# Kernel tuning notes

Hardware: AMD Instinct MI355X
Metric: run time of the kernel (lower is better)

The kernel has to match this reference:

```python
import jax, jax.numpy as jnp
import numpy as np

B, C, W, H = 16, 512, 32, 32


def spatial_shift1(y):
    # y: [B, W, H, C]; quartile-wise shifts with edge rows/cols left unchanged
    c = y.shape[-1]
    cq = c // 4
    p0 = jnp.concatenate([y[:, :1, :, 0*cq:1*cq], y[:, :-1, :, 0*cq:1*cq]], axis=1)  # w <- w-1
    p1 = jnp.concatenate([y[:, 1:, :, 1*cq:2*cq], y[:, -1:, :, 1*cq:2*cq]], axis=1)  # w <- w+1
    p2 = jnp.concatenate([y[:, :, :1, 2*cq:3*cq], y[:, :, :-1, 2*cq:3*cq]], axis=2)  # h <- h-1
    p3 = jnp.concatenate([y[:, :, 1:, 3*cq:], y[:, :, -1:, 3*cq:]], axis=2)          # h <- h+1
    return jnp.concatenate([p0, p1, p2, p3], axis=-1)


def spatial_shift2(y):
    # same as shift1 with w/h roles swapped
    c = y.shape[-1]
    cq = c // 4
    p0 = jnp.concatenate([y[:, :, :1, 0*cq:1*cq], y[:, :, :-1, 0*cq:1*cq]], axis=2)  # h <- h-1
    p1 = jnp.concatenate([y[:, :, 1:, 1*cq:2*cq], y[:, :, -1:, 1*cq:2*cq]], axis=2)  # h <- h+1
    p2 = jnp.concatenate([y[:, :1, :, 2*cq:3*cq], y[:, :-1, :, 2*cq:3*cq]], axis=1)  # w <- w-1
    p3 = jnp.concatenate([y[:, 1:, :, 3*cq:], y[:, -1:, :, 3*cq:]], axis=1)          # w <- w+1
    return jnp.concatenate([p0, p1, p2, p3], axis=-1)


def setup_inputs() -> dict:
    key = jax.random.key(0)
    ks = jax.random.split(key, 9)
    s = 0.02
    return {
        "x": jax.random.normal(ks[0], (B, C, W, H), dtype=jnp.float32),
        "w1": jax.random.normal(ks[1], (3 * C, C), dtype=jnp.float32) * s,
        "b1": jax.random.normal(ks[2], (3 * C,), dtype=jnp.float32) * s,
        "wa": jax.random.normal(ks[3], (C, C), dtype=jnp.float32) * s,
        "ba": jax.random.normal(ks[4], (C,), dtype=jnp.float32) * s,
        "wb": jax.random.normal(ks[5], (3 * C, C), dtype=jnp.float32) * s,
        "bb": jax.random.normal(ks[6], (3 * C,), dtype=jnp.float32) * s,
        "w2": jax.random.normal(ks[7], (C, C), dtype=jnp.float32) * s,
        "b2": jax.random.normal(ks[8], (C,), dtype=jnp.float32) * s,
    }


def reference(x, w1, b1, wa, ba, wb, bb, w2, b2):
    c = x.shape[1]
    xp = jnp.transpose(x, (0, 2, 3, 1))                     # [B, W, H, C]
    y = jnp.einsum("bwhc,oc->bwho", xp, w1) + b1            # [B, W, H, 3C]
    x1 = spatial_shift1(y[..., :c])
    x2 = spatial_shift2(y[..., c:2 * c])
    x3 = y[..., 2 * c:]
    # SplitAttention: descriptor a = sum over branches and spatial positions
    a = jnp.sum(x1 + x2 + x3, axis=(1, 2))                  # [B, C]
    hat = jax.nn.gelu(a @ wa.T + ba, approximate=False) @ wb.T + bb  # [B, 3C]
    bar = jax.nn.softmax(hat.reshape(-1, 3, c), axis=1)     # softmax over k=3
    g = bar[:, :, None, None, :]                            # [B, 3, 1, 1, C]
    out = g[:, 0] * x1 + g[:, 1] * x2 + g[:, 2] * x3        # [B, W, H, C]
    z = jnp.einsum("bwhc,oc->bwho", out, w2) + b2           # [B, W, H, C]
    return jnp.transpose(z, (0, 3, 1, 2))                   # [B, C, W, H]
```

## Files before the change

### kernel.cpp

```cpp
#include <hip/hip_runtime.h>
#include <stdint.h>

typedef __bf16 bf16x8 __attribute__((ext_vector_type(8)));
typedef float f32x4 __attribute__((ext_vector_type(4)));

#define B_ 16
#define C_ 512
#define S_ 1024
#define N1 1536

__device__ inline unsigned short f2b(float f) {
    unsigned int u = __builtin_bit_cast(unsigned int, f);
    unsigned int lsb = (u >> 16) & 1u;
    u += 0x7fffu + lsb;
    return (unsigned short)(u >> 16);
}
__device__ inline float b2f(unsigned int s) {
    unsigned int u = (s & 0xffffu) << 16;
    return __builtin_bit_cast(float, u);
}

__device__ inline void gl_lds16(const unsigned short* g, unsigned short* l) {
    __builtin_amdgcn_global_load_lds(
        (const __attribute__((address_space(1))) void*)(g),
        (__attribute__((address_space(3))) void*)(l),
        16, 0, 0);
}

__global__ __launch_bounds__(256) void transpose_convert_x(
    const float* __restrict__ x, unsigned short* __restrict__ xT,
    const float* __restrict__ w1, const float* __restrict__ w2,
    unsigned short* __restrict__ w1b, unsigned short* __restrict__ w2b,
    float* __restrict__ sums)
{
    int t = threadIdx.x;
    if (blockIdx.z == 16) {
        int base = (blockIdx.y * 16 + blockIdx.x) * 256 + t;
        for (int i = base; i < 292864; i += 32768) {
            if (i < 196608) {
                float4 v = ((const float4*)w1)[i];
                ((ushort4*)w1b)[i] = make_ushort4(f2b(v.x), f2b(v.y), f2b(v.z), f2b(v.w));
            } else if (i < 262144) {
                int j = i - 196608;
                float4 v = ((const float4*)w2)[j];
                ((ushort4*)w2b)[j] = make_ushort4(f2b(v.x), f2b(v.y), f2b(v.z), f2b(v.w));
            } else {
                int j = i - 262144;
                ((float4*)sums)[j] = make_float4(0.f, 0.f, 0.f, 0.f);
            }
        }
        return;
    }
    __shared__ float tile[64][68];
    int b = blockIdx.z;
    int c0 = blockIdx.y * 64;
    int s0 = blockIdx.x * 64;
    int r = t >> 2, q4 = t & 3;
    const float* xp = x + ((size_t)(b * C_ + c0 + r)) * S_ + s0;
#pragma unroll
    for (int k = 0; k < 4; k++) {
        float4 v = ((const float4*)xp)[q4 + 4 * k];
        *(float4*)&tile[r][(q4 + 4 * k) * 4] = v;
    }
    __syncthreads();
    int sr = t >> 2;
    unsigned short* op = xT + ((size_t)(b * S_ + s0 + sr)) * C_ + c0;
#pragma unroll
    for (int kk = 0; kk < 2; kk++) {
        int chunk = q4 + 4 * kk;
        unsigned int pz[4];
#pragma unroll
        for (int i2 = 0; i2 < 4; i2++) {
            int c = chunk * 8 + i2 * 2;
            pz[i2] = (unsigned int)f2b(tile[c][sr]) | ((unsigned int)f2b(tile[c + 1][sr]) << 16);
        }
        *(uint4*)&op[chunk * 8] = make_uint4(pz[0], pz[1], pz[2], pz[3]);
    }
}

template <bool TRANS_OUT, bool DO_SUMS>
__global__ __launch_bounds__(512, 2) void gemm_2ph(
    const unsigned short* __restrict__ A,
    const unsigned short* __restrict__ Wt,
    const float* __restrict__ bias,
    void* __restrict__ Cout,
    float* __restrict__ Tsum, float* __restrict__ H0, float* __restrict__ H31,
    float* __restrict__ C0, float* __restrict__ C31)
{
    __shared__ __align__(16) unsigned short lds[49152];
    const int tid = threadIdx.x;
    const int lane = tid & 63, wid = tid >> 6;
    const int wm = (wid >> 2) * 64;
    const int wn = (wid & 3) * 64;
    const int quad = lane >> 4, l16 = lane & 15;
    const int m0 = blockIdx.x * 128;
    const int n0 = blockIdx.y * 256;
    const unsigned short* Ab = A + (size_t)m0 * 512;
    const unsigned short* Bb = Wt + (size_t)n0 * 512;

    f32x4 acc[4][4] = {};

    auto stageA = [&](int T) {
        unsigned short* dst = &lds[(T & 1) * 8192];
#pragma unroll
        for (int i = 0; i < 2; i++) {
            int ch = i * 512 + tid;
            int r = ch >> 3, kc = ch & 7;
            gl_lds16(Ab + (size_t)r * 512 + T * 64 + ((kc ^ (r & 7)) * 8), dst + ch * 8);
        }
    };
    auto stageB = [&](int T) {
        unsigned short* dst = &lds[16384 + (T & 1) * 16384];
#pragma unroll
        for (int i = 0; i < 4; i++) {
            int ch = i * 512 + tid;
            int r = ch >> 3, kc = ch & 7;
            gl_lds16(Bb + (size_t)r * 512 + T * 64 + ((kc ^ (r & 7)) * 8), dst + ch * 8);
        }
    };

    stageB(0); stageA(0); stageB(1);
    asm volatile("s_waitcnt vmcnt(4)" ::: "memory");
    __builtin_amdgcn_s_barrier();

    for (int T = 0; T < 8; T++) {
        const unsigned short* Asl = &lds[(T & 1) * 8192];
        const unsigned short* Bsl = &lds[16384 + (T & 1) * 16384];
        bf16x8 bfr[4][2], af[2][2];
#pragma unroll
        for (int nt = 0; nt < 4; nt++)
#pragma unroll
            for (int kh = 0; kh < 2; kh++) {
                int rb = wn + nt * 16 + l16;
                bfr[nt][kh] = *(const bf16x8*)&Bsl[rb * 64 + (((kh * 4 + quad) ^ (rb & 7)) * 8)];
            }
#pragma unroll
        for (int mi = 0; mi < 2; mi++)
#pragma unroll
            for (int kh = 0; kh < 2; kh++) {
                int ra = wm + mi * 16 + l16;
                af[mi][kh] = *(const bf16x8*)&Asl[ra * 64 + (((kh * 4 + quad) ^ (ra & 7)) * 8)];
            }
        if (T < 7) stageA(T + 1);
        __builtin_amdgcn_s_barrier();
        asm volatile("s_waitcnt lgkmcnt(0)" ::: "memory");
        __builtin_amdgcn_sched_barrier(0);
        __builtin_amdgcn_s_setprio(1);
#pragma unroll
        for (int mi = 0; mi < 2; mi++)
#pragma unroll
            for (int nt = 0; nt < 4; nt++)
#pragma unroll
                for (int kh = 0; kh < 2; kh++)
                    acc[mi][nt] = __builtin_amdgcn_mfma_f32_16x16x32_bf16(
                        af[mi][kh], bfr[nt][kh], acc[mi][nt], 0, 0, 0);
        __builtin_amdgcn_s_setprio(0);
        __builtin_amdgcn_s_barrier();
#pragma unroll
        for (int mi = 0; mi < 2; mi++)
#pragma unroll
            for (int kh = 0; kh < 2; kh++) {
                int ra = wm + (2 + mi) * 16 + l16;
                af[mi][kh] = *(const bf16x8*)&Asl[ra * 64 + (((kh * 4 + quad) ^ (ra & 7)) * 8)];
            }
        if (T < 6) {
            stageB(T + 2);
            asm volatile("s_waitcnt vmcnt(4)" ::: "memory");
        } else if (T == 6) {
            asm volatile("s_waitcnt vmcnt(0)" ::: "memory");
        }
        __builtin_amdgcn_s_barrier();
        asm volatile("s_waitcnt lgkmcnt(0)" ::: "memory");
        __builtin_amdgcn_sched_barrier(0);
        __builtin_amdgcn_s_setprio(1);
#pragma unroll
        for (int mi = 0; mi < 2; mi++)
#pragma unroll
            for (int nt = 0; nt < 4; nt++)
#pragma unroll
                for (int kh = 0; kh < 2; kh++)
                    acc[2 + mi][nt] = __builtin_amdgcn_mfma_f32_16x16x32_bf16(
                        af[mi][kh], bfr[nt][kh], acc[2 + mi][nt], 0, 0, 0);
        __builtin_amdgcn_s_setprio(0);
        __builtin_amdgcn_s_barrier();
    }

    if (!TRANS_OUT) {
        unsigned short* eb = lds;
#pragma unroll
        for (int mt = 0; mt < 4; mt++)
#pragma unroll
            for (int nt = 0; nt < 4; nt++) {
                int col = wn + nt * 16 + l16;
                float bv = bias[n0 + col];
                int cc = col >> 3, cw = col & 7;
#pragma unroll
                for (int r = 0; r < 4; r++) {
                    int row = wm + mt * 16 + quad * 4 + r;
                    eb[row * 256 + (((cc ^ (row & 7)) << 3) + cw)] = f2b(acc[mt][nt][r] + bv);
                }
            }
        __syncthreads();
        unsigned short* Y = (unsigned short*)Cout;
#pragma unroll
        for (int it = 0; it < 8; it++) {
            int cid = it * 512 + tid;
            int row = cid >> 5, j = cid & 31;
            bf16x8 v = *(const bf16x8*)&eb[row * 256 + ((j ^ (row & 7)) << 3)];
            *(bf16x8*)&Y[(size_t)(m0 + row) * N1 + n0 + j * 8] = v;
        }
    } else {
        float* ef = (float*)lds;
        int b = m0 >> 10, s0r = m0 & 1023;
        float* O = (float*)Cout;
#pragma unroll
        for (int p = 0; p < 2; p++) {
            if (((wid & 3) >> 1) == p) {
#pragma unroll
                for (int mt = 0; mt < 4; mt++)
#pragma unroll
                    for (int nt = 0; nt < 4; nt++) {
                        int nl = wn - p * 128 + nt * 16 + l16;
                        float bv = bias[n0 + p * 128 + nl];
                        int c = (wm >> 2) + mt * 4 + quad;
                        f32x4 v;
#pragma unroll
                        for (int r = 0; r < 4; r++) v[r] = acc[mt][nt][r] + bv;
                        *(f32x4*)&ef[nl * 128 + ((c ^ (nl & 7)) << 2)] = v;
                    }
            }
            __syncthreads();
#pragma unroll
            for (int it = 0; it < 8; it++) {
                int cid = it * 512 + tid;
                int nl = cid >> 5, j = cid & 31;
                f32x4 v = *(const f32x4*)&ef[nl * 128 + ((j ^ (nl & 7)) << 2)];
                *(f32x4*)&O[((size_t)(b * 512 + n0 + p * 128 + nl)) * 1024 + s0r + j * 4] = v;
            }
            if (p == 0) __syncthreads();
        }
    }

    if (DO_SUMS) {
        int b = m0 >> 10;
        int wlo = (m0 & 1023) >> 5;
#pragma unroll
        for (int nt = 0; nt < 4; nt++) {
            int n = n0 + wn + nt * 16 + l16;
            float bv = bias[n];
            float tT = 0.f;
#pragma unroll
            for (int mt = 0; mt < 4; mt++)
#pragma unroll
                for (int r = 0; r < 4; r++) tT += acc[mt][nt][r] + bv;
            tT += __shfl_xor(tT, 16);
            tT += __shfl_xor(tT, 32);
            if (quad == 0) {
                atomicAdd(&Tsum[b * 1536 + n], tT);
                float th0 = acc[0][nt][0] + acc[2][nt][0] + 2.f * bv;
                atomicAdd(&H0[b * 1536 + n], th0);
            }
            if (quad == 3) {
                float th31 = acc[1][nt][3] + acc[3][nt][3] + 2.f * bv;
                atomicAdd(&H31[b * 1536 + n], th31);
            }
            if (wlo == 0 && wm == 0) {
                float tc = 0.f;
#pragma unroll
                for (int mt = 0; mt < 2; mt++)
#pragma unroll
                    for (int r = 0; r < 4; r++) tc += acc[mt][nt][r] + bv;
                tc += __shfl_xor(tc, 16);
                tc += __shfl_xor(tc, 32);
                if (quad == 0) atomicAdd(&C0[b * 1536 + n], tc);
            }
            if (wlo == 28 && wm == 64) {
                float tc = 0.f;
#pragma unroll
                for (int mt = 2; mt < 4; mt++)
#pragma unroll
                    for (int r = 0; r < 4; r++) tc += acc[mt][nt][r] + bv;
                tc += __shfl_xor(tc, 16);
                tc += __shfl_xor(tc, 32);
                if (quad == 0) atomicAdd(&C31[b * 1536 + n], tc);
            }
        }
    }
}

__global__ __launch_bounds__(512, 2) void gemm2_fused(
    const unsigned short* __restrict__ Yg,
    const float* __restrict__ hat,
    const unsigned short* __restrict__ Wt,
    const float* __restrict__ bias,
    float* __restrict__ O)
{
    __shared__ __align__(16) unsigned short As[2 * 8192];
    __shared__ __align__(16) unsigned short Bs[2 * 16384];
    __shared__ float gs[3][512];
    const int tid = threadIdx.x;
    const int lane = tid & 63, wid = tid >> 6;
    const int wm = (wid >> 2) * 64;
    const int wn = (wid & 3) * 64;
    const int quad = lane >> 4, l16 = lane & 15;
    const int m0 = blockIdx.x * 128;
    const int n0 = blockIdx.y * 256;
    const int b = m0 >> 10, s0 = m0 & 1023, w0 = s0 >> 5;
    const int bq = b * 1024;
    const unsigned short* Bb = Wt + (size_t)n0 * 512;
    const int chunk = tid & 7, mpair = tid >> 3;
    const int wA = w0 + ((mpair * 2) >> 5);

    f32x4 acc[4][4] = {};

    {
        int c = tid;
        float h0v = hat[b * 1536 + c];
        float h1v = hat[b * 1536 + 512 + c];
        float h2v = hat[b * 1536 + 1024 + c];
        float mx = fmaxf(h0v, fmaxf(h1v, h2v));
        float e0 = __expf(h0v - mx), e1 = __expf(h1v - mx), e2 = __expf(h2v - mx);
        float inv = 1.0f / (e0 + e1 + e2);
        gs[0][c] = e0 * inv; gs[1][c] = e1 * inv; gs[2][c] = e2 * inv;
    }
    __syncthreads();

    auto stageB = [&](int T) {
        unsigned short* dst = &Bs[(T & 1) * 16384];
#pragma unroll
        for (int i = 0; i < 4; i++) {
            int ch = i * 512 + tid;
            int r = ch >> 3, kc = ch & 7;
            gl_lds16(Bb + (size_t)r * 512 + T * 64 + ((kc ^ (r & 7)) * 8), dst + ch * 8);
        }
    };

    uint4 u1[2], u2[2], u3[2];
    auto issueA = [&](int Tn) {
        int q = Tn >> 1;
        int dw1 = (q == 0) ? -1 : (q == 1) ? 1 : 0;
        int dh1 = (q == 2) ? -1 : (q == 3) ? 1 : 0;
        int dh2 = (q == 0) ? -1 : (q == 1) ? 1 : 0;
        int dw2 = (q == 2) ? -1 : (q == 3) ? 1 : 0;
        int cg = Tn * 64 + chunk * 8;
#pragma unroll
        for (int j = 0; j < 2; j++) {
            int ml = mpair * 2 + j;
            int w = w0 + (ml >> 5), h = ml & 31;
            int r1 = bq + min(max(w + dw1, 0), 31) * 32 + min(max(h + dh1, 0), 31);
            int r2 = bq + min(max(w + dw2, 0), 31) * 32 + min(max(h + dh2, 0), 31);
            int r3 = bq + w * 32 + h;
            u1[j] = *(const uint4*)&Yg[(size_t)r1 * 1536 + cg];
            u2[j] = *(const uint4*)&Yg[(size_t)r2 * 1536 + 512 + cg];
            u3[j] = *(const uint4*)&Yg[(size_t)r3 * 1536 + 1024 + cg];
        }
    };
    auto writeA = [&](int Tn) {
        int cg = Tn * 64 + chunk * 8;
        float g0v[8], g1v[8], g2v[8];
        *(float4*)&g0v[0] = *(const float4*)&gs[0][cg];
        *(float4*)&g0v[4] = *(const float4*)&gs[0][cg + 4];
        *(float4*)&g1v[0] = *(const float4*)&gs[1][cg];
        *(float4*)&g1v[4] = *(const float4*)&gs[1][cg + 4];
        *(float4*)&g2v[0] = *(const float4*)&gs[2][cg];
        *(float4*)&g2v[4] = *(const float4*)&gs[2][cg + 4];
#pragma unroll
        for (int j = 0; j < 2; j++) {
            const unsigned int* a1 = (const unsigned int*)&u1[j];
            const unsigned int* a2 = (const unsigned int*)&u2[j];
            const unsigned int* a3 = (const unsigned int*)&u3[j];
            unsigned int p[4];
#pragma unroll
            for (int k = 0; k < 4; k++) {
                float lo = g0v[2 * k] * b2f(a1[k]) + g1v[2 * k] * b2f(a2[k]) + g2v[2 * k] * b2f(a3[k]);
                float hi = g0v[2 * k + 1] * b2f(a1[k] >> 16) + g1v[2 * k + 1] * b2f(a2[k] >> 16) + g2v[2 * k + 1] * b2f(a3[k] >> 16);
                p[k] = (unsigned int)f2b(lo) | ((unsigned int)f2b(hi) << 16);
            }
            int ml = mpair * 2 + j;
            *(uint4*)&As[(Tn & 1) * 8192 + ml * 64 + ((chunk ^ (ml & 7)) * 8)] = *(const uint4*)p;
        }
    };

    stageB(0);
    issueA(0);
    stageB(1);
    asm volatile("s_waitcnt vmcnt(4)" ::: "memory");
    writeA(0);
    asm volatile("s_waitcnt lgkmcnt(0)" ::: "memory");
    __builtin_amdgcn_s_barrier();

    for (int T = 0; T < 8; T++) {
        const unsigned short* Asl = &As[(T & 1) * 8192];
        const unsigned short* Bsl = &Bs[(T & 1) * 16384];
        bf16x8 bfr[4][2], af[2][2];
#pragma unroll
        for (int nt = 0; nt < 4; nt++)
#pragma unroll
            for (int kh = 0; kh < 2; kh++) {
                int rb = wn + nt * 16 + l16;
                bfr[nt][kh] = *(const bf16x8*)&Bsl[rb * 64 + (((kh * 4 + quad) ^ (rb & 7)) * 8)];
            }
#pragma unroll
        for (int mi = 0; mi < 2; mi++)
#pragma unroll
            for (int kh = 0; kh < 2; kh++) {
                int ra = wm + mi * 16 + l16;
                af[mi][kh] = *(const bf16x8*)&Asl[ra * 64 + (((kh * 4 + quad) ^ (ra & 7)) * 8)];
            }
        if (T < 7) issueA(T + 1);
        __builtin_amdgcn_s_barrier();
        asm volatile("s_waitcnt lgkmcnt(0)" ::: "memory");
        __builtin_amdgcn_sched_barrier(0);
        __builtin_amdgcn_s_setprio(1);
#pragma unroll
        for (int mi = 0; mi < 2; mi++)
#pragma unroll
            for (int nt = 0; nt < 4; nt++)
#pragma unroll
                for (int kh = 0; kh < 2; kh++)
                    acc[mi][nt] = __builtin_amdgcn_mfma_f32_16x16x32_bf16(
                        af[mi][kh], bfr[nt][kh], acc[mi][nt], 0, 0, 0);
        __builtin_amdgcn_s_setprio(0);
        __builtin_amdgcn_s_barrier();
#pragma unroll
        for (int mi = 0; mi < 2; mi++)
#pragma unroll
            for (int kh = 0; kh < 2; kh++) {
                int ra = wm + (2 + mi) * 16 + l16;
                af[mi][kh] = *(const bf16x8*)&Asl[ra * 64 + (((kh * 4 + quad) ^ (ra & 7)) * 8)];
            }
        if (T < 6) stageB(T + 2);
        if (T < 7) {
            if (T < 6) asm volatile("s_waitcnt vmcnt(4)" ::: "memory");
            else       asm volatile("s_waitcnt vmcnt(0)" ::: "memory");
            writeA(T + 1);
        }
        __builtin_amdgcn_s_barrier();
        asm volatile("s_waitcnt lgkmcnt(0)" ::: "memory");
        __builtin_amdgcn_sched_barrier(0);
        __builtin_amdgcn_s_setprio(1);
#pragma unroll
        for (int mi = 0; mi < 2; mi++)
#pragma unroll
            for (int nt = 0; nt < 4; nt++)
#pragma unroll
                for (int kh = 0; kh < 2; kh++)
                    acc[2 + mi][nt] = __builtin_amdgcn_mfma_f32_16x16x32_bf16(
                        af[mi][kh], bfr[nt][kh], acc[2 + mi][nt], 0, 0, 0);
        __builtin_amdgcn_s_setprio(0);
        __builtin_amdgcn_s_barrier();
    }

    float* ef = (float*)Bs;
#pragma unroll
    for (int p = 0; p < 2; p++) {
        if (((wid & 3) >> 1) == p) {
#pragma unroll
            for (int mt = 0; mt < 4; mt++)
#pragma unroll
                for (int nt = 0; nt < 4; nt++) {
                    int nl = wn - p * 128 + nt * 16 + l16;
                    float bv = bias[n0 + p * 128 + nl];
                    int c = (wm >> 2) + mt * 4 + quad;
                    f32x4 v;
#pragma unroll
                    for (int r = 0; r < 4; r++) v[r] = acc[mt][nt][r] + bv;
                    *(f32x4*)&ef[nl * 128 + ((c ^ (nl & 7)) << 2)] = v;
                }
        }
        __syncthreads();
#pragma unroll
        for (int it = 0; it < 8; it++) {
            int cid = it * 512 + tid;
            int nl = cid >> 5, j = cid & 31;
            f32x4 v = *(const f32x4*)&ef[nl * 128 + ((j ^ (nl & 7)) << 2)];
            *(f32x4*)&O[((size_t)(b * 512 + n0 + p * 128 + nl)) * 1024 + s0 + j * 4] = v;
        }
        if (p == 0) __syncthreads();
    }
}

__global__ __launch_bounds__(256) void mlp_layer1(
    const float* __restrict__ sums, const float* __restrict__ wa,
    const float* __restrict__ ba, float* __restrict__ h)
{
    __shared__ float sa[512];
    int b = blockIdx.x >> 7;
    int t = threadIdx.x;
    const float* Tp   = sums;
    const float* H0p  = sums + 24576;
    const float* H31p = sums + 49152;
    const float* C0p  = sums + 73728;
    const float* C31p = sums + 98304;
#pragma unroll
    for (int j = 0; j < 2; j++) {
        int c = t + j * 256;
        int q = c >> 7;
        int n1 = b * 1536 + c;
        float t123 = Tp[n1] + Tp[n1 + 512] + Tp[n1 + 1024];
        float sC1 = C0p[n1] - C31p[n1];
        float sH1 = H0p[n1] - H31p[n1];
        float sC2 = C0p[n1 + 512] - C31p[n1 + 512];
        float sH2 = H0p[n1 + 512] - H31p[n1 + 512];
        float e = (q < 2) ? (sC1 + sH2) : (sH1 + sC2);
        sa[c] = t123 + ((q & 1) ? -e : e);
    }
    __syncthreads();
    int lane = t & 63, wid = t >> 6;
    int o = (blockIdx.x & 127) * 4 + wid;
    const float4* wr = (const float4*)(wa + (size_t)o * 512);
    float4 w0 = wr[lane * 2], w1v = wr[lane * 2 + 1];
    float4 a0 = ((const float4*)sa)[lane * 2], a1 = ((const float4*)sa)[lane * 2 + 1];
    float dot = w0.x * a0.x + w0.y * a0.y + w0.z * a0.z + w0.w * a0.w
              + w1v.x * a1.x + w1v.y * a1.y + w1v.z * a1.z + w1v.w * a1.w;
#pragma unroll
    for (int off = 32; off; off >>= 1) dot += __shfl_down(dot, off);
    if (lane == 0) {
        float v = dot + ba[o];
        h[b * 512 + o] = 0.5f * v * (1.0f + erff(v * 0.7071067811865475f));
    }
}

__global__ __launch_bounds__(256) void mlp_layer2(
    const float* __restrict__ h, const float* __restrict__ wb,
    const float* __restrict__ bb, float* __restrict__ hat)
{
    __shared__ float sh[512];
    int b = blockIdx.x / 96;
    int og = blockIdx.x - b * 96;
    int t = threadIdx.x;
    sh[t] = h[b * 512 + t];
    sh[t + 256] = h[b * 512 + 256 + t];
    __syncthreads();
    int lane = t & 63, wid = t >> 6;
    float4 a0 = ((const float4*)sh)[lane * 2], a1 = ((const float4*)sh)[lane * 2 + 1];
#pragma unroll
    for (int i = 0; i < 4; i++) {
        int o = og * 16 + wid * 4 + i;
        const float4* wr = (const float4*)(wb + (size_t)o * 512);
        float4 w0 = wr[lane * 2], w1 = wr[lane * 2 + 1];
        float dot = w0.x * a0.x + w0.y * a0.y + w0.z * a0.z + w0.w * a0.w
                  + w1.x * a1.x + w1.y * a1.y + w1.z * a1.z + w1.w * a1.w;
#pragma unroll
        for (int off = 32; off; off >>= 1) dot += __shfl_down(dot, off);
        if (lane == 0)
            hat[(size_t)b * 1536 + o] = dot + bb[o];
    }
}

extern "C" void kernel_launch(void* const* d_in, const int* in_sizes, int n_in,
                              void* d_out, int out_size, void* d_ws, size_t ws_size,
                              hipStream_t stream) {
    const float* x  = (const float*)d_in[0];
    const float* w1 = (const float*)d_in[1];
    const float* b1 = (const float*)d_in[2];
    const float* wa = (const float*)d_in[3];
    const float* ba = (const float*)d_in[4];
    const float* wb = (const float*)d_in[5];
    const float* bb = (const float*)d_in[6];
    const float* w2 = (const float*)d_in[7];
    const float* b2 = (const float*)d_in[8];
    float* out = (float*)d_out;

    char* ws = (char*)d_ws;
    unsigned short* xT   = (unsigned short*)(ws);
    unsigned short* w1b  = (unsigned short*)(ws + 16777216);
    unsigned short* w2b  = (unsigned short*)(ws + 18350080);
    unsigned short* y    = (unsigned short*)(ws + 18874368);
    float* sums          = (float*)(ws + 69206016);
    float* h_buf         = (float*)(ws + 69697536);
    float* hat_buf       = (float*)(ws + 69730304);

    float* Tsum = sums;
    float* H0   = sums + 24576;
    float* H31  = sums + 49152;
    float* C0   = sums + 73728;
    float* C31  = sums + 98304;

    transpose_convert_x<<<dim3(16, 8, 17), dim3(256), 0, stream>>>(
        x, xT, w1, w2, w1b, w2b, sums);
    gemm_2ph<false, true><<<dim3(128, 6), dim3(512), 0, stream>>>(
        xT, w1b, b1, (void*)y, Tsum, H0, H31, C0, C31);
    mlp_layer1<<<dim3(2048), dim3(256), 0, stream>>>(sums, wa, ba, h_buf);
    mlp_layer2<<<dim3(1536), dim3(256), 0, stream>>>(h_buf, wb, bb, hat_buf);
    gemm2_fused<<<dim3(128, 2), dim3(512), 0, stream>>>(
        y, hat_buf, w2b, b2, out);
}
```

Baseline: 175.3 us.

## Rewrite first GEMM with 128x128 tiles and register double-buffered fragments

The first projection GEMM moves from 128x256 tiles with 512 threads to 128x128 tiles with 256 threads. The grid becomes 12x128 with N as the fast dimension, so neighbouring blocks share the same A rows. A and B are staged together into LDS two tiles ahead. The next tile's MFMA fragments are preloaded into a second register buffer while the current tile's MFMAs run, to overlap LDS reads with compute. The cost is more register pressure and a full vmcnt(0) wait plus a barrier every iteration, which may cut into the overlap.

```diff
diff --git a/kernel.cpp b/kernel.cpp
--- a/kernel.cpp
+++ b/kernel.cpp
@@ -78,114 +78,93 @@
     }
 }
 
-template <bool TRANS_OUT, bool DO_SUMS>
-__global__ __launch_bounds__(512, 2) void gemm_2ph(
+__global__ __launch_bounds__(256, 2) void gemm1_sb(
     const unsigned short* __restrict__ A,
     const unsigned short* __restrict__ Wt,
     const float* __restrict__ bias,
-    void* __restrict__ Cout,
+    unsigned short* __restrict__ Y,
     float* __restrict__ Tsum, float* __restrict__ H0, float* __restrict__ H31,
     float* __restrict__ C0, float* __restrict__ C31)
 {
-    __shared__ __align__(16) unsigned short lds[49152];
+    __shared__ __align__(16) unsigned short lds[32768];
     const int tid = threadIdx.x;
     const int lane = tid & 63, wid = tid >> 6;
-    const int wm = (wid >> 2) * 64;
-    const int wn = (wid & 3) * 64;
+    const int wm = (wid >> 1) * 64;
+    const int wn = (wid & 1) * 64;
     const int quad = lane >> 4, l16 = lane & 15;
-    const int m0 = blockIdx.x * 128;
-    const int n0 = blockIdx.y * 256;
+    const int n0 = blockIdx.x * 128;
+    const int m0 = blockIdx.y * 128;
     const unsigned short* Ab = A + (size_t)m0 * 512;
     const unsigned short* Bb = Wt + (size_t)n0 * 512;
 
     f32x4 acc[4][4] = {};
-
-    auto stageA = [&](int T) {
-        unsigned short* dst = &lds[(T & 1) * 8192];
-#pragma unroll
-        for (int i = 0; i < 2; i++) {
-            int ch = i * 512 + tid;
+    bf16x8 afs[2][4][2], bfs[2][4][2];
+
+    auto stage = [&](int T) {
+        unsigned short* dA = &lds[(T & 1) * 8192];
+        unsigned short* dB = &lds[16384 + (T & 1) * 8192];
+#pragma unroll
+        for (int i = 0; i < 4; i++) {
+            int ch = i * 256 + tid;
             int r = ch >> 3, kc = ch & 7;
-            gl_lds16(Ab + (size_t)r * 512 + T * 64 + ((kc ^ (r & 7)) * 8), dst + ch * 8);
+            size_t go = (size_t)r * 512 + T * 64 + ((kc ^ (r & 7)) * 8);
+            gl_lds16(Ab + go, dA + ch * 8);
+            gl_lds16(Bb + go, dB + ch * 8);
         }
     };
-    auto stageB = [&](int T) {
-        unsigned short* dst = &lds[16384 + (T & 1) * 16384];
-#pragma unroll
-        for (int i = 0; i < 4; i++) {
-            int ch = i * 512 + tid;
-            int r = ch >> 3, kc = ch & 7;
-            gl_lds16(Bb + (size_t)r * 512 + T * 64 + ((kc ^ (r & 7)) * 8), dst + ch * 8);
-        }
-    };
-
-    stageB(0); stageA(0); stageB(1);
-    asm volatile("s_waitcnt vmcnt(4)" ::: "memory");
+
+    stage(0); stage(1);
+    asm volatile("s_waitcnt vmcnt(8)" ::: "memory");
     __builtin_amdgcn_s_barrier();
-
+    {
+        const unsigned short* Asl = &lds[0];
+        const unsigned short* Bsl = &lds[16384];
+#pragma unroll
+        for (int mt = 0; mt < 4; mt++)
+#pragma unroll
+            for (int kh = 0; kh < 2; kh++) {
+                int ra = wm + mt * 16 + l16;
+                afs[0][mt][kh] = *(const bf16x8*)&Asl[ra * 64 + (((kh * 4 + quad) ^ (ra & 7)) * 8)];
+                int rb = wn + mt * 16 + l16;
+                bfs[0][mt][kh] = *(const bf16x8*)&Bsl[rb * 64 + (((kh * 4 + quad) ^ (rb & 7)) * 8)];
+            }
+    }
+
+#pragma unroll
     for (int T = 0; T < 8; T++) {
-        const unsigned short* Asl = &lds[(T & 1) * 8192];
-        const unsigned short* Bsl = &lds[16384 + (T & 1) * 16384];
-        bf16x8 bfr[4][2], af[2][2];
-#pragma unroll
-        for (int nt = 0; nt < 4; nt++)
-#pragma unroll
-            for (int kh = 0; kh < 2; kh++) {
-                int rb = wn + nt * 16 + l16;
-                bfr[nt][kh] = *(const bf16x8*)&Bsl[rb * 64 + (((kh * 4 + quad) ^ (rb & 7)) * 8)];
-            }
-#pragma unroll
-        for (int mi = 0; mi < 2; mi++)
-#pragma unroll
-            for (int kh = 0; kh < 2; kh++) {
-                int ra = wm + mi * 16 + l16;
-                af[mi][kh] = *(const bf16x8*)&Asl[ra * 64 + (((kh * 4 + quad) ^ (ra & 7)) * 8)];
-            }
-        if (T < 7) stageA(T + 1);
+        const int cur = T & 1, nxt = cur ^ 1;
+        asm volatile("s_waitcnt lgkmcnt(0)" ::: "memory");
+        asm volatile("s_waitcnt vmcnt(0)" ::: "memory");
         __builtin_amdgcn_s_barrier();
-        asm volatile("s_waitcnt lgkmcnt(0)" ::: "memory");
+        if (T < 6) stage(T + 2);
+        if (T < 7) {
+            const unsigned short* Asl = &lds[nxt * 8192];
+            const unsigned short* Bsl = &lds[16384 + nxt * 8192];
+#pragma unroll
+            for (int mt = 0; mt < 4; mt++)
+#pragma unroll
+                for (int kh = 0; kh < 2; kh++) {
+                    int ra = wm + mt * 16 + l16;
+                    afs[nxt][mt][kh] = *(const bf16x8*)&Asl[ra * 64 + (((kh * 4 + quad) ^ (ra & 7)) * 8)];
+                    int rb = wn + mt * 16 + l16;
+                    bfs[nxt][mt][kh] = *(const bf16x8*)&Bsl[rb * 64 + (((kh * 4 + quad) ^ (rb & 7)) * 8)];
+                }
+        }
         __builtin_amdgcn_sched_barrier(0);
         __builtin_amdgcn_s_setprio(1);
 #pragma unroll
-        for (int mi = 0; mi < 2; mi++)
+        for (int mt = 0; mt < 4; mt++)
 #pragma unroll
             for (int nt = 0; nt < 4; nt++)
 #pragma unroll
                 for (int kh = 0; kh < 2; kh++)
-                    acc[mi][nt] = __builtin_amdgcn_mfma_f32_16x16x32_bf16(
-                        af[mi][kh], bfr[nt][kh], acc[mi][nt], 0, 0, 0);
+                    acc[mt][nt] = __builtin_amdgcn_mfma_f32_16x16x32_bf16(
+                        afs[cur][mt][kh], bfs[cur][nt][kh], acc[mt][nt], 0, 0, 0);
         __builtin_amdgcn_s_setprio(0);
-        __builtin_amdgcn_s_barrier();
-#pragma unroll
-        for (int mi = 0; mi < 2; mi++)
-#pragma unroll
-            for (int kh = 0; kh < 2; kh++) {
-                int ra = wm + (2 + mi) * 16 + l16;
-                af[mi][kh] = *(const bf16x8*)&Asl[ra * 64 + (((kh * 4 + quad) ^ (ra & 7)) * 8)];
-            }
-        if (T < 6) {
-            stageB(T + 2);
-            asm volatile("s_waitcnt vmcnt(4)" ::: "memory");
-        } else if (T == 6) {
-            asm volatile("s_waitcnt vmcnt(0)" ::: "memory");
-        }
-        __builtin_amdgcn_s_barrier();
-        asm volatile("s_waitcnt lgkmcnt(0)" ::: "memory");
-        __builtin_amdgcn_sched_barrier(0);
-        __builtin_amdgcn_s_setprio(1);
-#pragma unroll
-        for (int mi = 0; mi < 2; mi++)
-#pragma unroll
-            for (int nt = 0; nt < 4; nt++)
-#pragma unroll
-                for (int kh = 0; kh < 2; kh++)
-                    acc[2 + mi][nt] = __builtin_amdgcn_mfma_f32_16x16x32_bf16(
-                        af[mi][kh], bfr[nt][kh], acc[2 + mi][nt], 0, 0, 0);
-        __builtin_amdgcn_s_setprio(0);
-        __builtin_amdgcn_s_barrier();
-    }
-
-    if (!TRANS_OUT) {
+    }
+    __syncthreads();
+
+    {
         unsigned short* eb = lds;
 #pragma unroll
         for (int mt = 0; mt < 4; mt++)
@@ -197,51 +176,20 @@
 #pragma unroll
                 for (int r = 0; r < 4; r++) {
                     int row = wm + mt * 16 + quad * 4 + r;
-                    eb[row * 256 + (((cc ^ (row & 7)) << 3) + cw)] = f2b(acc[mt][nt][r] + bv);
+                    eb[row * 128 + (((cc ^ (row & 7)) << 3) + cw)] = f2b(acc[mt][nt][r] + bv);
                 }
             }
         __syncthreads();
-        unsigned short* Y = (unsigned short*)Cout;
 #pragma unroll
         for (int it = 0; it < 8; it++) {
-            int cid = it * 512 + tid;
-            int row = cid >> 5, j = cid & 31;
-            bf16x8 v = *(const bf16x8*)&eb[row * 256 + ((j ^ (row & 7)) << 3)];
+            int cid = it * 256 + tid;
+            int row = cid >> 4, j = cid & 15;
+            bf16x8 v = *(const bf16x8*)&eb[row * 128 + ((j ^ (row & 7)) << 3)];
             *(bf16x8*)&Y[(size_t)(m0 + row) * N1 + n0 + j * 8] = v;
         }
-    } else {
-        float* ef = (float*)lds;
-        int b = m0 >> 10, s0r = m0 & 1023;
-        float* O = (float*)Cout;
-#pragma unroll
-        for (int p = 0; p < 2; p++) {
-            if (((wid & 3) >> 1) == p) {
-#pragma unroll
-                for (int mt = 0; mt < 4; mt++)
-#pragma unroll
-                    for (int nt = 0; nt < 4; nt++) {
-                        int nl = wn - p * 128 + nt * 16 + l16;
-                        float bv = bias[n0 + p * 128 + nl];
-                        int c = (wm >> 2) + mt * 4 + quad;
-                        f32x4 v;
-#pragma unroll
-                        for (int r = 0; r < 4; r++) v[r] = acc[mt][nt][r] + bv;
-                        *(f32x4*)&ef[nl * 128 + ((c ^ (nl & 7)) << 2)] = v;
-                    }
-            }
-            __syncthreads();
-#pragma unroll
-            for (int it = 0; it < 8; it++) {
-                int cid = it * 512 + tid;
-                int nl = cid >> 5, j = cid & 31;
-                f32x4 v = *(const f32x4*)&ef[nl * 128 + ((j ^ (nl & 7)) << 2)];
-                *(f32x4*)&O[((size_t)(b * 512 + n0 + p * 128 + nl)) * 1024 + s0r + j * 4] = v;
-            }
-            if (p == 0) __syncthreads();
-        }
-    }
-
-    if (DO_SUMS) {
+    }
+
+    {
         int b = m0 >> 10;
         int wlo = (m0 & 1023) >> 5;
 #pragma unroll
@@ -309,7 +257,6 @@
     const int bq = b * 1024;
     const unsigned short* Bb = Wt + (size_t)n0 * 512;
     const int chunk = tid & 7, mpair = tid >> 3;
-    const int wA = w0 + ((mpair * 2) >> 5);
 
     f32x4 acc[4][4] = {};
 
@@ -579,8 +526,8 @@
 
     transpose_convert_x<<<dim3(16, 8, 17), dim3(256), 0, stream>>>(
         x, xT, w1, w2, w1b, w2b, sums);
-    gemm_2ph<false, true><<<dim3(128, 6), dim3(512), 0, stream>>>(
-        xT, w1b, b1, (void*)y, Tsum, H0, H31, C0, C31);
+    gemm1_sb<<<dim3(12, 128), dim3(256), 0, stream>>>(
+        xT, w1b, b1, y, Tsum, H0, H31, C0, C31);
     mlp_layer1<<<dim3(2048), dim3(256), 0, stream>>>(sums, wa, ba, h_buf);
     mlp_layer2<<<dim3(1536), dim3(256), 0, stream>>>(h_buf, wb, bb, hat_buf);
     gemm2_fused<<<dim3(128, 2), dim3(512), 0, stream>>>(
```

Result: slower. 179.8 us (+2.6%).
